# Performance work log

Measured on AMD Instinct MI355X. Metric: run time of the kernel, lower is better.

## Reference

```python
import jax, jax.numpy as jnp
import numpy as np

N_NODES = 20000
N_EDGES = 320000
N_GRAPHS = 256
F_IN = 128
HID = 512


def _xavier(key, shape, gain=1.0):
    fan_out, fan_in = shape
    a = gain * np.sqrt(6.0 / (fan_in + fan_out))
    return jax.random.uniform(key, shape, jnp.float32, -a, a)


def setup_inputs() -> dict:
    key = jax.random.key(0)
    ks = jax.random.split(key, 9)
    x = jax.random.normal(ks[0], (N_NODES, F_IN), jnp.float32)
    edge_index = jax.random.randint(ks[1], (2, N_EDGES), 0, N_NODES, dtype=jnp.int64)
    batch = jnp.sort(jax.random.randint(ks[2], (N_NODES,), 0, N_GRAPHS, dtype=jnp.int64))
    return {
        "x": x,
        "edge_index": edge_index,
        "batch": batch,
        "lin_W": _xavier(ks[3], (HID, F_IN)),
        "lin_b": jnp.zeros((HID,), jnp.float32),
        "W1": _xavier(ks[4], (HID, F_IN)),
        "b1": jnp.zeros((HID,), jnp.float32),
        "W2": _xavier(ks[5], (HID, HID)),
        "b2": jnp.zeros((HID,), jnp.float32),
        "W3": _xavier(ks[6], (HID, HID)),
        "b3": jnp.zeros((HID,), jnp.float32),
        "W4": _xavier(ks[7], (HID, HID)),
        "b4": jnp.zeros((HID,), jnp.float32),
    }


def _gcn_conv(x, W, b, src, dst, norm, n_nodes):
    # PyG GCNConv: h = x @ W.T; out_i = sum_j norm_ij * h_j (scatter over dst) + b
    h = x @ W.T
    msg = h[src] * norm[:, None]  # [E', H] gather + scale
    return jax.ops.segment_sum(msg, dst, num_segments=n_nodes) + b


def reference(x, edge_index, batch, lin_W, lin_b, W1, b1, W2, b2, W3, b3, W4, b4):
    n = x.shape[0]
    loop = jnp.arange(n, dtype=edge_index.dtype)
    src = jnp.concatenate([edge_index[0], loop])
    dst = jnp.concatenate([edge_index[1], loop])
    # symmetric normalization D^-1/2 (A+I) D^-1/2, degree = in-degree over dst
    deg = jax.ops.segment_sum(jnp.ones_like(src, dtype=x.dtype), dst, num_segments=n)
    dis = jnp.where(deg > 0, jax.lax.rsqrt(deg), 0.0)
    norm = dis[src] * dis[dst]

    x_l = x @ lin_W.T + lin_b  # dead code when act=None (kept for faithfulness)

    h1 = _gcn_conv(x, W1, b1, src, dst, norm, n)
    h2 = _gcn_conv(h1, W2, b2, src, dst, norm, n)
    h3 = _gcn_conv(h2, W3, b3, src, dst, norm, n)
    h4 = _gcn_conv(h3, W4, b4, src, dst, norm, n)
    h = jnp.concatenate([h1, h2, h3, h4], axis=1)  # [N, 4*HID]

    h_pooled = jax.ops.segment_max(h, batch, num_segments=N_GRAPHS)
    h_pos = (h > 0).astype(h.dtype)
    counts = jax.ops.segment_sum(jnp.ones((n,), h.dtype), batch, num_segments=N_GRAPHS)
    h_pos_pooled = jax.ops.segment_sum(h_pos, batch, num_segments=N_GRAPHS) / jnp.maximum(counts, 1.0)[:, None]
    return jnp.concatenate([h_pooled, h_pos_pooled], axis=1)  # [G, 8*HID]
```

## Files before the change

kernel.cpp:

```cpp
#include <hip/hip_runtime.h>
#include <cfloat>
#include <cmath>

#define F_IN 128
#define HID 512

typedef short bf16x8 __attribute__((ext_vector_type(8)));
typedef float f32x4 __attribute__((ext_vector_type(4)));

__device__ static inline void split_bf16(float v, short& hi, short& lo) {
    unsigned u = __float_as_uint(v);
    unsigned r = u + 0x7FFF + ((u >> 16) & 1);
    hi = (short)(r >> 16);
    float hf = __uint_as_float(((unsigned)(unsigned short)hi) << 16);
    float res = v - hf;
    unsigned u2 = __float_as_uint(res);
    unsigned r2 = u2 + 0x7FFF + ((u2 >> 16) & 1);
    lo = (short)(r2 >> 16);
}

__device__ static inline void gload_lds16(const void* g, void* l) {
    __builtin_amdgcn_global_load_lds(
        (const __attribute__((address_space(1))) unsigned int*)g,
        (__attribute__((address_space(3))) unsigned int*)l,
        16, 0, 0);
}


__global__ void zero_kernel(int* __restrict__ a, int n) {
    int i = blockIdx.x * blockDim.x + threadIdx.x;
    if (i < n) a[i] = 0;
}

__global__ void count_in_kernel(const int* __restrict__ dst, int* __restrict__ cnt, int E) {
    int e = blockIdx.x * blockDim.x + threadIdx.x;
    if (e < E) atomicAdd(&cnt[dst[e]], 1);
}

__global__ void scan_kernel(const int* __restrict__ cnt, int* __restrict__ offs, int n) {
    __shared__ int buf[1024];
    __shared__ int carry_s;
    if (threadIdx.x == 0) carry_s = 0;
    __syncthreads();
    for (int base = 0; base < n; base += 1024) {
        int i = base + threadIdx.x;
        int v = (i < n) ? cnt[i] : 0;
        buf[threadIdx.x] = v;
        __syncthreads();
        for (int s = 1; s < 1024; s <<= 1) {
            int t = (threadIdx.x >= s) ? buf[threadIdx.x - s] : 0;
            __syncthreads();
            buf[threadIdx.x] += t;
            __syncthreads();
        }
        int total = buf[1023];
        if (i < n) offs[i] = carry_s + buf[threadIdx.x] - v;
        __syncthreads();
        if (threadIdx.x == 0) carry_s += total;
        __syncthreads();
    }
    if (threadIdx.x == 0) offs[n] = carry_s;
}

__global__ void dis_kernel(const int* __restrict__ offs, float* __restrict__ dis, int n) {
    int i = blockIdx.x * blockDim.x + threadIdx.x;
    if (i < n) dis[i] = rsqrtf((float)(offs[i + 1] - offs[i] + 1));
}

__global__ void fill_csr_kernel(const int* __restrict__ src, const int* __restrict__ dst,
                                const int* __restrict__ offs, int* __restrict__ cursor,
                                unsigned short* __restrict__ csr, int E) {
    int e = blockIdx.x * blockDim.x + threadIdx.x;
    if (e < E) {
        int d = dst[e];
        int p = atomicAdd(&cursor[d], 1);
        csr[offs[d] + p] = (unsigned short)src[e];
    }
}

__global__ void starts_kernel(const int* __restrict__ batch, int* __restrict__ starts,
                              int n, int G) {
    int i = blockIdx.x * blockDim.x + threadIdx.x;
    if (i >= n) return;
    int b = batch[i];
    if (i == 0) {
        for (int g = 0; g <= b; g++) starts[g] = 0;
    } else {
        int bp = batch[i - 1];
        for (int g = bp + 1; g <= b; g++) starts[g] = i;
    }
    if (i == n - 1) {
        for (int g = b + 1; g <= G; g++) starts[g] = n;
    }
}

__global__ void wconv_kernel(const float* __restrict__ W, short* __restrict__ Whi,
                             short* __restrict__ Wlo, int n) {
    int i = blockIdx.x * blockDim.x + threadIdx.x;
    if (i < n) {
        short h, l;
        split_bf16(W[i], h, l);
        Whi[i] = h;
        Wlo[i] = l;
    }
}


__global__ void agg_f128_kernel(const float* __restrict__ X, const float* __restrict__ dis,
                                const int* __restrict__ offs, const unsigned short* __restrict__ csr,
                                short* __restrict__ Ahi, short* __restrict__ Alo, int n) {
    int i = blockIdx.x;
    int t = threadIdx.x;
    const float2* X2 = (const float2*)X;
    float di = dis[i];
    float2 h = X2[(size_t)i * 64 + t];
    float ax = di * h.x, ay = di * h.y;
    int e = offs[i], e1 = offs[i + 1];
    for (; e + 4 <= e1; e += 4) {
        int j0 = csr[e], j1 = csr[e + 1], j2 = csr[e + 2], j3 = csr[e + 3];
        float d0 = dis[j0], d1 = dis[j1], d2 = dis[j2], d3 = dis[j3];
        float2 r0 = X2[(size_t)j0 * 64 + t];
        float2 r1 = X2[(size_t)j1 * 64 + t];
        float2 r2 = X2[(size_t)j2 * 64 + t];
        float2 r3 = X2[(size_t)j3 * 64 + t];
        ax += d0 * r0.x + d1 * r1.x + d2 * r2.x + d3 * r3.x;
        ay += d0 * r0.y + d1 * r1.y + d2 * r2.y + d3 * r3.y;
    }
    for (; e < e1; e++) {
        int j = csr[e];
        float d = dis[j];
        float2 r = X2[(size_t)j * 64 + t];
        ax += d * r.x;
        ay += d * r.y;
    }
    ax *= di; ay *= di;
    short hx, lx, hy, ly;
    split_bf16(ax, hx, lx);
    split_bf16(ay, hy, ly);
    *(short2*)&Ahi[(size_t)i * F_IN + t * 2] = make_short2(hx, hy);
    *(short2*)&Alo[(size_t)i * F_IN + t * 2] = make_short2(lx, ly);
}

__global__ void agg_f512_kernel(const float* __restrict__ H, const float* __restrict__ dis,
                                const int* __restrict__ offs, const unsigned short* __restrict__ csr,
                                short* __restrict__ Ahi, short* __restrict__ Alo, int n) {
    int i = blockIdx.x;
    int t = threadIdx.x;
    const float4* H4 = (const float4*)H;
    float di = dis[i];
    float4 h = H4[(size_t)i * 128 + t];
    float ax = di * h.x, ay = di * h.y, az = di * h.z, aw = di * h.w;
    int e = offs[i], e1 = offs[i + 1];
    for (; e + 4 <= e1; e += 4) {
        int j0 = csr[e], j1 = csr[e + 1], j2 = csr[e + 2], j3 = csr[e + 3];
        float d0 = dis[j0], d1 = dis[j1], d2 = dis[j2], d3 = dis[j3];
        float4 r0 = H4[(size_t)j0 * 128 + t];
        float4 r1 = H4[(size_t)j1 * 128 + t];
        float4 r2 = H4[(size_t)j2 * 128 + t];
        float4 r3 = H4[(size_t)j3 * 128 + t];
        ax += d0 * r0.x + d1 * r1.x + d2 * r2.x + d3 * r3.x;
        ay += d0 * r0.y + d1 * r1.y + d2 * r2.y + d3 * r3.y;
        az += d0 * r0.z + d1 * r1.z + d2 * r2.z + d3 * r3.z;
        aw += d0 * r0.w + d1 * r1.w + d2 * r2.w + d3 * r3.w;
    }
    for (; e < e1; e++) {
        int j = csr[e];
        float d = dis[j];
        float4 r = H4[(size_t)j * 128 + t];
        ax += d * r.x;
        ay += d * r.y;
        az += d * r.z;
        aw += d * r.w;
    }
    ax *= di; ay *= di; az *= di; aw *= di;
    short h0, l0, h1, l1, h2, l2, h3, l3;
    split_bf16(ax, h0, l0);
    split_bf16(ay, h1, l1);
    split_bf16(az, h2, l2);
    split_bf16(aw, h3, l3);
    *(short4*)&Ahi[(size_t)i * HID + t * 4] = make_short4(h0, h1, h2, h3);
    *(short4*)&Alo[(size_t)i * HID + t * 4] = make_short4(l0, l1, l2, l3);
}

__global__ __launch_bounds__(256) void gemm_mfma_kernel(
    const short* __restrict__ Ahi, const short* __restrict__ Alo,
    const short* __restrict__ Whi, const short* __restrict__ Wlo,
    const float* __restrict__ bias, float* __restrict__ C,
    int M, int K, int Nout) {
    __shared__ __attribute__((aligned(16))) short lds[4][4096];

    int tid = threadIdx.x;
    int w = tid >> 6, l = tid & 63;
    int m0 = blockIdx.x * 128, n0 = blockIdx.y * 128;
    int lrow = l & 15, lq = l >> 4;

    const short* gp = (w == 0) ? Ahi : (w == 1) ? Alo : (w == 2) ? Whi : Wlo;
    int base_mn = (w < 2) ? m0 : n0;

    f32x4 acc[4][4];
    #pragma unroll
    for (int i = 0; i < 4; i++)
        #pragma unroll
        for (int j = 0; j < 4; j++) acc[i][j] = (f32x4){0.f, 0.f, 0.f, 0.f};

    int wm = w >> 1, wn = w & 1;

    for (int k0 = 0; k0 < K; k0 += 32) {
        const short* gbase = gp + (size_t)(base_mn + lrow) * K + (k0 + lq * 8);
        #pragma unroll
        for (int s = 0; s < 8; s++) {
            gload_lds16(gbase + (size_t)s * 16 * K, &lds[w][s * 64 * 8]);
        }
        __syncthreads();

        bf16x8 ah[4], al[4], wh[4], wl[4];
        #pragma unroll
        for (int i = 0; i < 4; i++) {
            int sA = wm * 4 + i;
            ah[i] = *(const bf16x8*)&lds[0][(sA * 64 + l) * 8];
            al[i] = *(const bf16x8*)&lds[1][(sA * 64 + l) * 8];
            int sW = wn * 4 + i;
            wh[i] = *(const bf16x8*)&lds[2][(sW * 64 + l) * 8];
            wl[i] = *(const bf16x8*)&lds[3][(sW * 64 + l) * 8];
        }
        #pragma unroll
        for (int i = 0; i < 4; i++)
            #pragma unroll
            for (int j = 0; j < 4; j++) {
                acc[i][j] = __builtin_amdgcn_mfma_f32_16x16x32_bf16(ah[i], wh[j], acc[i][j], 0, 0, 0);
                acc[i][j] = __builtin_amdgcn_mfma_f32_16x16x32_bf16(ah[i], wl[j], acc[i][j], 0, 0, 0);
                acc[i][j] = __builtin_amdgcn_mfma_f32_16x16x32_bf16(al[i], wh[j], acc[i][j], 0, 0, 0);
            }
        __syncthreads();
    }

    #pragma unroll
    for (int j = 0; j < 4; j++) {
        int col = n0 + (wn * 4 + j) * 16 + lrow;
        float bv = bias[col];
        #pragma unroll
        for (int i = 0; i < 4; i++) {
            int mrow = m0 + (wm * 4 + i) * 16 + lq * 4;
            #pragma unroll
            for (int r = 0; r < 4; r++) {
                int mm = mrow + r;
                if (mm < M) C[(size_t)mm * Nout + col] = acc[i][j][r] + bv;
            }
        }
    }
}

__global__ void pool_kernel(const float* __restrict__ H, const int* __restrict__ starts,
                            float* __restrict__ out, int layer) {
    int g = blockIdx.x;
    int c = blockIdx.y * 256 + threadIdx.x;
    int s = starts[g], e = starts[g + 1];
    float mx = -INFINITY;
    int pos = 0;
    #pragma unroll 4
    for (int n = s; n < e; n++) {
        float v = H[(size_t)n * HID + c];
        mx = fmaxf(mx, v);
        pos += (v > 0.0f) ? 1 : 0;
    }
    float cntf = fmaxf((float)(e - s), 1.0f);
    out[(size_t)g * (8 * HID) + layer * HID + c] = mx;
    out[(size_t)g * (8 * HID) + 4 * HID + layer * HID + c] = (float)pos / cntf;
}

extern "C" void kernel_launch(void* const* d_in, const int* in_sizes, int n_in,
                              void* d_out, int out_size, void* d_ws, size_t ws_size,
                              hipStream_t stream) {
    const float* x     = (const float*)d_in[0];
    const int*   eidx  = (const int*)d_in[1];
    const int*   batch = (const int*)d_in[2];
    const float* W1 = (const float*)d_in[5];
    const float* b1 = (const float*)d_in[6];
    const float* W2 = (const float*)d_in[7];
    const float* b2 = (const float*)d_in[8];
    const float* W3 = (const float*)d_in[9];
    const float* b3 = (const float*)d_in[10];
    const float* W4 = (const float*)d_in[11];
    const float* b4 = (const float*)d_in[12];
    float* out = (float*)d_out;

    const int N = in_sizes[0] / F_IN;
    const int E = in_sizes[1] / 2;
    const int G = out_size / (8 * HID);

    const int* src = eidx;
    const int* dst = eidx + E;

    char* w = (char*)d_ws;
    short* Ahi = (short*)w; w += (size_t)N * HID * sizeof(short);
    short* Alo = (short*)w; w += (size_t)N * HID * sizeof(short);
    float* H   = (float*)w; w += (size_t)N * HID * sizeof(float);
    short* Whi = (short*)w; w += (size_t)HID * HID * sizeof(short);
    short* Wlo = (short*)w; w += (size_t)HID * HID * sizeof(short);
    int* offs  = (int*)w;   w += (size_t)(N + 4) * sizeof(int);
    unsigned short* csr = (unsigned short*)w; w += (size_t)E * sizeof(unsigned short);
    int* cnt   = (int*)w;   w += (size_t)N * sizeof(int);
    float* dis = (float*)w; w += (size_t)N * sizeof(float);
    int* starts = (int*)w;  w += (size_t)(G + 1) * sizeof(int);

    const int TB = 256;
    zero_kernel<<<(N + TB - 1) / TB, TB, 0, stream>>>(cnt, N);
    count_in_kernel<<<(E + TB - 1) / TB, TB, 0, stream>>>(dst, cnt, E);
    scan_kernel<<<1, 1024, 0, stream>>>(cnt, offs, N);
    dis_kernel<<<(N + TB - 1) / TB, TB, 0, stream>>>(offs, dis, N);
    zero_kernel<<<(N + TB - 1) / TB, TB, 0, stream>>>(cnt, N);
    fill_csr_kernel<<<(E + TB - 1) / TB, TB, 0, stream>>>(src, dst, offs, cnt, csr, E);
    starts_kernel<<<(N + TB - 1) / TB, TB, 0, stream>>>(batch, starts, N, G);

    dim3 gemm_grid((N + 127) / 128, HID / 128);
    dim3 pool_grid(G, HID / 256);

    wconv_kernel<<<(HID * F_IN + TB - 1) / TB, TB, 0, stream>>>(W1, Whi, Wlo, HID * F_IN);
    agg_f128_kernel<<<N, 64, 0, stream>>>(x, dis, offs, csr, Ahi, Alo, N);
    gemm_mfma_kernel<<<gemm_grid, 256, 0, stream>>>(Ahi, Alo, Whi, Wlo, b1, H, N, F_IN, HID);
    pool_kernel<<<pool_grid, 256, 0, stream>>>(H, starts, out, 0);

    const float* Ws_[3] = {W2, W3, W4};
    const float* bs_[3] = {b2, b3, b4};
    for (int ll = 0; ll < 3; ll++) {
        wconv_kernel<<<(HID * HID + TB - 1) / TB, TB, 0, stream>>>(Ws_[ll], Whi, Wlo, HID * HID);
        agg_f512_kernel<<<N, 128, 0, stream>>>(H, dis, offs, csr, Ahi, Alo, N);
        gemm_mfma_kernel<<<gemm_grid, 256, 0, stream>>>(Ahi, Alo, Whi, Wlo, bs_[ll], H, N, HID, HID);
        pool_kernel<<<pool_grid, 256, 0, stream>>>(H, starts, out, ll + 1);
    }
}
```

Before: 733.3 us.

## Split aggregation into 64-column chunks and batch weight conversion

The per-node aggregation kernels are replaced by one templated kernel that launches a block per 64-column chunk of each node, so each thread loads a single float per neighbor and the edge loop is unrolled to 8. All four weight matrices are now converted to bf16 hi/lo in a single launch into a larger workspace, and the CSR fill counts down from the degree counts instead of re-zeroing a cursor. This removes several small launches and gives many more small blocks for latency hiding. The cost is that each neighbor's index and dis value are re-read once per chunk, and each load is narrower (float instead of float4).

```diff
diff --git a/kernel.cpp b/kernel.cpp
--- a/kernel.cpp
+++ b/kernel.cpp
@@ -68,13 +68,13 @@
 }
 
 __global__ void fill_csr_kernel(const int* __restrict__ src, const int* __restrict__ dst,
-                                const int* __restrict__ offs, int* __restrict__ cursor,
+                                const int* __restrict__ offs, int* __restrict__ cnt,
                                 unsigned short* __restrict__ csr, int E) {
     int e = blockIdx.x * blockDim.x + threadIdx.x;
     if (e < E) {
         int d = dst[e];
-        int p = atomicAdd(&cursor[d], 1);
-        csr[offs[d] + p] = (unsigned short)src[e];
+        int p = atomicSub(&cnt[d], 1);
+        csr[offs[d] + p - 1] = (unsigned short)src[e];
     }
 }
 
@@ -94,92 +94,58 @@
     }
 }
 
-__global__ void wconv_kernel(const float* __restrict__ W, short* __restrict__ Whi,
-                             short* __restrict__ Wlo, int n) {
+__global__ void wconv_kernel(const float* __restrict__ W1, const float* __restrict__ W2,
+                             const float* __restrict__ W3, const float* __restrict__ W4,
+                             short* __restrict__ Whi, short* __restrict__ Wlo) {
     int i = blockIdx.x * blockDim.x + threadIdx.x;
-    if (i < n) {
-        short h, l;
-        split_bf16(W[i], h, l);
-        Whi[i] = h;
-        Wlo[i] = l;
-    }
-}
-
-
-__global__ void agg_f128_kernel(const float* __restrict__ X, const float* __restrict__ dis,
-                                const int* __restrict__ offs, const unsigned short* __restrict__ csr,
-                                short* __restrict__ Ahi, short* __restrict__ Alo, int n) {
-    int i = blockIdx.x;
-    int t = threadIdx.x;
-    const float2* X2 = (const float2*)X;
+    const int n1 = HID * F_IN, nk = HID * HID;
+    float v;
+    if (i < n1) v = W1[i];
+    else if (i < n1 + nk) v = W2[i - n1];
+    else if (i < n1 + 2 * nk) v = W3[i - n1 - nk];
+    else if (i < n1 + 3 * nk) v = W4[i - n1 - 2 * nk];
+    else return;
+    short h, l;
+    split_bf16(v, h, l);
+    Whi[i] = h;
+    Wlo[i] = l;
+}
+
+template <int F, int CHUNKS>
+__global__ __launch_bounds__(64) void agg_chunk_kernel(
+    const float* __restrict__ H, const float* __restrict__ dis,
+    const int* __restrict__ offs, const unsigned short* __restrict__ csr,
+    short* __restrict__ Ahi, short* __restrict__ Alo, int n) {
+    int blk = blockIdx.x;
+    int i = blk / CHUNKS;
+    int chunk = blk % CHUNKS;
+    int col = chunk * 64 + threadIdx.x;
+    const float* Hc = H + col;
+
     float di = dis[i];
-    float2 h = X2[(size_t)i * 64 + t];
-    float ax = di * h.x, ay = di * h.y;
+    float a = di * Hc[(size_t)i * F];
     int e = offs[i], e1 = offs[i + 1];
-    for (; e + 4 <= e1; e += 4) {
-        int j0 = csr[e], j1 = csr[e + 1], j2 = csr[e + 2], j3 = csr[e + 3];
+    for (; e + 8 <= e1; e += 8) {
+        int j0 = csr[e],     j1 = csr[e + 1], j2 = csr[e + 2], j3 = csr[e + 3];
+        int j4 = csr[e + 4], j5 = csr[e + 5], j6 = csr[e + 6], j7 = csr[e + 7];
         float d0 = dis[j0], d1 = dis[j1], d2 = dis[j2], d3 = dis[j3];
-        float2 r0 = X2[(size_t)j0 * 64 + t];
-        float2 r1 = X2[(size_t)j1 * 64 + t];
-        float2 r2 = X2[(size_t)j2 * 64 + t];
-        float2 r3 = X2[(size_t)j3 * 64 + t];
-        ax += d0 * r0.x + d1 * r1.x + d2 * r2.x + d3 * r3.x;
-        ay += d0 * r0.y + d1 * r1.y + d2 * r2.y + d3 * r3.y;
+        float d4 = dis[j4], d5 = dis[j5], d6 = dis[j6], d7 = dis[j7];
+        float r0 = Hc[(size_t)j0 * F], r1 = Hc[(size_t)j1 * F];
+        float r2 = Hc[(size_t)j2 * F], r3 = Hc[(size_t)j3 * F];
+        float r4 = Hc[(size_t)j4 * F], r5 = Hc[(size_t)j5 * F];
+        float r6 = Hc[(size_t)j6 * F], r7 = Hc[(size_t)j7 * F];
+        a += d0 * r0 + d1 * r1 + d2 * r2 + d3 * r3;
+        a += d4 * r4 + d5 * r5 + d6 * r6 + d7 * r7;
     }
     for (; e < e1; e++) {
         int j = csr[e];
-        float d = dis[j];
-        float2 r = X2[(size_t)j * 64 + t];
-        ax += d * r.x;
-        ay += d * r.y;
-    }
-    ax *= di; ay *= di;
-    short hx, lx, hy, ly;
-    split_bf16(ax, hx, lx);
-    split_bf16(ay, hy, ly);
-    *(short2*)&Ahi[(size_t)i * F_IN + t * 2] = make_short2(hx, hy);
-    *(short2*)&Alo[(size_t)i * F_IN + t * 2] = make_short2(lx, ly);
-}
-
-__global__ void agg_f512_kernel(const float* __restrict__ H, const float* __restrict__ dis,
-                                const int* __restrict__ offs, const unsigned short* __restrict__ csr,
-                                short* __restrict__ Ahi, short* __restrict__ Alo, int n) {
-    int i = blockIdx.x;
-    int t = threadIdx.x;
-    const float4* H4 = (const float4*)H;
-    float di = dis[i];
-    float4 h = H4[(size_t)i * 128 + t];
-    float ax = di * h.x, ay = di * h.y, az = di * h.z, aw = di * h.w;
-    int e = offs[i], e1 = offs[i + 1];
-    for (; e + 4 <= e1; e += 4) {
-        int j0 = csr[e], j1 = csr[e + 1], j2 = csr[e + 2], j3 = csr[e + 3];
-        float d0 = dis[j0], d1 = dis[j1], d2 = dis[j2], d3 = dis[j3];
-        float4 r0 = H4[(size_t)j0 * 128 + t];
-        float4 r1 = H4[(size_t)j1 * 128 + t];
-        float4 r2 = H4[(size_t)j2 * 128 + t];
-        float4 r3 = H4[(size_t)j3 * 128 + t];
-        ax += d0 * r0.x + d1 * r1.x + d2 * r2.x + d3 * r3.x;
-        ay += d0 * r0.y + d1 * r1.y + d2 * r2.y + d3 * r3.y;
-        az += d0 * r0.z + d1 * r1.z + d2 * r2.z + d3 * r3.z;
-        aw += d0 * r0.w + d1 * r1.w + d2 * r2.w + d3 * r3.w;
-    }
-    for (; e < e1; e++) {
-        int j = csr[e];
-        float d = dis[j];
-        float4 r = H4[(size_t)j * 128 + t];
-        ax += d * r.x;
-        ay += d * r.y;
-        az += d * r.z;
-        aw += d * r.w;
-    }
-    ax *= di; ay *= di; az *= di; aw *= di;
-    short h0, l0, h1, l1, h2, l2, h3, l3;
-    split_bf16(ax, h0, l0);
-    split_bf16(ay, h1, l1);
-    split_bf16(az, h2, l2);
-    split_bf16(aw, h3, l3);
-    *(short4*)&Ahi[(size_t)i * HID + t * 4] = make_short4(h0, h1, h2, h3);
-    *(short4*)&Alo[(size_t)i * HID + t * 4] = make_short4(l0, l1, l2, l3);
+        a += dis[j] * Hc[(size_t)j * F];
+    }
+    a *= di;
+    short h, l;
+    split_bf16(a, h, l);
+    Ahi[(size_t)i * F + col] = h;
+    Alo[(size_t)i * F + col] = l;
 }
 
 __global__ __launch_bounds__(256) void gemm_mfma_kernel(
@@ -291,41 +257,45 @@
     const int* src = eidx;
     const int* dst = eidx + E;
 
+    const size_t nW = (size_t)HID * F_IN + 3 * (size_t)HID * HID;
     char* w = (char*)d_ws;
     short* Ahi = (short*)w; w += (size_t)N * HID * sizeof(short);
     short* Alo = (short*)w; w += (size_t)N * HID * sizeof(short);
     float* H   = (float*)w; w += (size_t)N * HID * sizeof(float);
-    short* Whi = (short*)w; w += (size_t)HID * HID * sizeof(short);
-    short* Wlo = (short*)w; w += (size_t)HID * HID * sizeof(short);
+    short* Whi = (short*)w; w += nW * sizeof(short);
+    short* Wlo = (short*)w; w += nW * sizeof(short);
     int* offs  = (int*)w;   w += (size_t)(N + 4) * sizeof(int);
     unsigned short* csr = (unsigned short*)w; w += (size_t)E * sizeof(unsigned short);
     int* cnt   = (int*)w;   w += (size_t)N * sizeof(int);
     float* dis = (float*)w; w += (size_t)N * sizeof(float);
     int* starts = (int*)w;  w += (size_t)(G + 1) * sizeof(int);
 
+    const size_t wo1 = 0;
+    const size_t wo2 = (size_t)HID * F_IN;
+    const size_t wo3 = wo2 + (size_t)HID * HID;
+    const size_t wo4 = wo3 + (size_t)HID * HID;
+
     const int TB = 256;
     zero_kernel<<<(N + TB - 1) / TB, TB, 0, stream>>>(cnt, N);
     count_in_kernel<<<(E + TB - 1) / TB, TB, 0, stream>>>(dst, cnt, E);
     scan_kernel<<<1, 1024, 0, stream>>>(cnt, offs, N);
     dis_kernel<<<(N + TB - 1) / TB, TB, 0, stream>>>(offs, dis, N);
-    zero_kernel<<<(N + TB - 1) / TB, TB, 0, stream>>>(cnt, N);
     fill_csr_kernel<<<(E + TB - 1) / TB, TB, 0, stream>>>(src, dst, offs, cnt, csr, E);
     starts_kernel<<<(N + TB - 1) / TB, TB, 0, stream>>>(batch, starts, N, G);
+    wconv_kernel<<<((int)nW + TB - 1) / TB, TB, 0, stream>>>(W1, W2, W3, W4, Whi, Wlo);
 
     dim3 gemm_grid((N + 127) / 128, HID / 128);
     dim3 pool_grid(G, HID / 256);
 
-    wconv_kernel<<<(HID * F_IN + TB - 1) / TB, TB, 0, stream>>>(W1, Whi, Wlo, HID * F_IN);
-    agg_f128_kernel<<<N, 64, 0, stream>>>(x, dis, offs, csr, Ahi, Alo, N);
-    gemm_mfma_kernel<<<gemm_grid, 256, 0, stream>>>(Ahi, Alo, Whi, Wlo, b1, H, N, F_IN, HID);
+    agg_chunk_kernel<F_IN, 2><<<N * 2, 64, 0, stream>>>(x, dis, offs, csr, Ahi, Alo, N);
+    gemm_mfma_kernel<<<gemm_grid, 256, 0, stream>>>(Ahi, Alo, Whi + wo1, Wlo + wo1, b1, H, N, F_IN, HID);
     pool_kernel<<<pool_grid, 256, 0, stream>>>(H, starts, out, 0);
 
-    const float* Ws_[3] = {W2, W3, W4};
+    const size_t wos[3] = {wo2, wo3, wo4};
     const float* bs_[3] = {b2, b3, b4};
     for (int ll = 0; ll < 3; ll++) {
-        wconv_kernel<<<(HID * HID + TB - 1) / TB, TB, 0, stream>>>(Ws_[ll], Whi, Wlo, HID * HID);
-        agg_f512_kernel<<<N, 128, 0, stream>>>(H, dis, offs, csr, Ahi, Alo, N);
-        gemm_mfma_kernel<<<gemm_grid, 256, 0, stream>>>(Ahi, Alo, Whi, Wlo, bs_[ll], H, N, HID, HID);
+        agg_chunk_kernel<HID, 8><<<N * 8, 64, 0, stream>>>(H, dis, offs, csr, Ahi, Alo, N);
+        gemm_mfma_kernel<<<gemm_grid, 256, 0, stream>>>(Ahi, Alo, Whi + wos[ll], Wlo + wos[ll], bs_[ll], H, N, HID, HID);
         pool_kernel<<<pool_grid, 256, 0, stream>>>(H, starts, out, ll + 1);
     }
 }
```

After: 686.2 us. 1.07x faster.
